# Kernel tuning notes

Hardware: AMD Instinct MI355X
Metric: run time of the kernel (lower is better)

The kernel has to match this reference:

```python
import jax, jax.numpy as jnp
import numpy as np

D_MODEL = 2048
D_COMPARE = 2048
D_MEMORY = 2048
N_HEADS = 16
KV_HEADS = 4
KV_REPEAT = N_HEADS // KV_HEADS          # 4
C_HD = D_COMPARE // N_HEADS              # 128 compare head dim
M_HD = D_MEMORY // N_HEADS               # 128 memory head dim
TOTAL_OUT = D_COMPARE + KV_HEADS * C_HD + KV_HEADS * M_HD  # 3072


def setup_inputs() -> dict:
    key = jax.random.key(0)
    ks = jax.random.split(key, 5)
    b, t = 2, 2048
    x = jax.random.normal(ks[0], (b, t, D_MODEL), dtype=jnp.float32)
    s_in = 1.0 / np.sqrt(D_MODEL)
    s_out = 1.0 / np.sqrt(D_MEMORY)
    in_w = jax.random.uniform(ks[1], (TOTAL_OUT, D_MODEL), jnp.float32, -s_in, s_in)
    in_b = jax.random.uniform(ks[2], (TOTAL_OUT,), jnp.float32, -s_in, s_in)
    out_w = jax.random.uniform(ks[3], (D_MODEL, D_MEMORY), jnp.float32, -s_out, s_out)
    out_b = jax.random.uniform(ks[4], (D_MODEL,), jnp.float32, -s_out, s_out)
    return {"x": x, "in_w": in_w, "in_b": in_b, "out_w": out_w, "out_b": out_b}


def reference(x, in_w, in_b, out_w, out_b):
    b, t, _ = x.shape
    packed = jnp.einsum("btd,od->bto", x, in_w) + in_b          # [b,t,TOTAL_OUT]
    q, k, v = jnp.split(packed, [D_COMPARE, D_COMPARE + KV_HEADS * C_HD], axis=-1)
    # q: [b, kv, rep, t, hd] -- head h maps to kv group h // KV_REPEAT
    # (torch repeat_interleave on KV head dim == grouped reshape of q heads)
    q = q.reshape(b, t, KV_HEADS, KV_REPEAT, C_HD).transpose(0, 2, 3, 1, 4)
    k = k.reshape(b, t, KV_HEADS, C_HD).transpose(0, 2, 1, 3)   # [b,kv,t,hd]
    v = v.reshape(b, t, KV_HEADS, M_HD).transpose(0, 2, 1, 3)   # [b,kv,t,mhd]
    scale = 1.0 / np.sqrt(C_HD)
    scores = jnp.einsum("bgrqd,bgkd->bgrqk", q, k) * scale      # [b,kv,rep,t,t]
    attn = jax.nn.softmax(scores, axis=-1)
    y = jnp.einsum("bgrqk,bgkd->bgrqd", attn, v)                # [b,kv,rep,t,mhd]
    y = y.transpose(0, 3, 1, 2, 4).reshape(b, t, D_MEMORY)      # heads back in order
    return jnp.einsum("btm,dm->btd", y, out_w) + out_b
```

## Files before the change

kernel.cpp:

```cpp
#include <hip/hip_runtime.h>
#include <hip/hip_bf16.h>
#include <stdint.h>

#define DEV __device__ __forceinline__

typedef __attribute__((ext_vector_type(8))) short bf16x8;
typedef __attribute__((ext_vector_type(4))) float f32x4;
typedef __attribute__((ext_vector_type(16))) float f32x16;
typedef __attribute__((ext_vector_type(4))) unsigned u32x4;

DEV unsigned short f2bf(float f) {
  unsigned u = __builtin_bit_cast(unsigned, f);
  unsigned r = u + 0x7FFF + ((u >> 16) & 1);
  return (unsigned short)(r >> 16);
}

DEV unsigned short f2bfh(float f) {
  __bf16 h = (__bf16)f;
  return __builtin_bit_cast(unsigned short, h);
}

DEV unsigned cvtpk(float lo, float hi) {
  unsigned r;
  asm("v_cvt_pk_bf16_f32 %0, %1, %2" : "=v"(r) : "v"(lo), "v"(hi));
  return r;
}

DEV void plswap(unsigned &a, unsigned &b) {
  asm("v_permlane32_swap_b32 %0, %1" : "+v"(a), "+v"(b));
}

typedef __attribute__((address_space(1))) void gvoid;
typedef __attribute__((address_space(3))) void lvoid;

DEV void g2l16(const void* g, void* l) {
  __builtin_amdgcn_global_load_lds((gvoid*)g, (lvoid*)l, 16, 0, 0);
}

#define MFMA16(a, b, c) __builtin_amdgcn_mfma_f32_16x16x32_bf16(a, b, c, 0, 0, 0)
#define MFMA32(a, b, c) __builtin_amdgcn_mfma_f32_32x32x16_bf16(a, b, c, 0, 0, 0)

__global__ void k_cvt3(const float* __restrict__ x, unsigned short* __restrict__ xo, int nx4,
                       const float* __restrict__ w, unsigned short* __restrict__ wo, int nw4,
                       const float* __restrict__ v, unsigned short* __restrict__ vo, int nv4) {
  int i = blockIdx.x * blockDim.x + threadIdx.x;
  int stride = gridDim.x * blockDim.x;
  int tot = nx4 + nw4 + nv4;
  for (; i < tot; i += stride) {
    const float* src; unsigned short* dst; int j = i;
    if (j < nx4) { src = x; dst = xo; }
    else if ((j -= nx4) < nw4) { src = w; dst = wo; }
    else { j -= nw4; src = v; dst = vo; }
    float4 val = reinterpret_cast<const float4*>(src)[j];
    ushort4 o;
    o.x = f2bf(val.x); o.y = f2bf(val.y); o.z = f2bf(val.z); o.w = f2bf(val.w);
    reinterpret_cast<ushort4*>(dst)[j] = o;
  }
}

template<bool BF16OUT>
__global__ __launch_bounds__(256, 2) void k_gemm(
    const unsigned short* __restrict__ A, const unsigned short* __restrict__ B,
    const float* __restrict__ bias, void* __restrict__ C,
    int M, int N, int K) {
  __shared__ unsigned short As[128 * 32];
  __shared__ unsigned short Bs[128 * 32];
  int tid = threadIdx.x;
  int lane = tid & 63, wid = tid >> 6;
  int bm = blockIdx.y * 128, bn = blockIdx.x * 128;
  int wm = (wid >> 1) * 64, wn = (wid & 1) * 64;
  int row16 = lane & 15, kq = lane >> 4;
  f32x4 acc[4][4] = {};
  int r = tid >> 2, c = (tid & 3) * 8;
  const unsigned short* Ag = A + (size_t)(bm + r) * K + c;
  const unsigned short* Bg = B + (size_t)(bn + r) * K + c;
  for (int k0 = 0; k0 < K; k0 += 32) {
    g2l16(Ag + k0, &As[tid * 8]);
    g2l16(Ag + (size_t)64 * K + k0, &As[2048 + tid * 8]);
    g2l16(Bg + k0, &Bs[tid * 8]);
    g2l16(Bg + (size_t)64 * K + k0, &Bs[2048 + tid * 8]);
    __syncthreads();
    bf16x8 a[4], b[4];
#pragma unroll
    for (int m = 0; m < 4; m++) a[m] = *(const bf16x8*)&As[(wm + m * 16 + row16) * 32 + kq * 8];
#pragma unroll
    for (int n = 0; n < 4; n++) b[n] = *(const bf16x8*)&Bs[(wn + n * 16 + row16) * 32 + kq * 8];
    __builtin_amdgcn_s_setprio(1);
#pragma unroll
    for (int m = 0; m < 4; m++)
#pragma unroll
      for (int n = 0; n < 4; n++)
        acc[m][n] = MFMA16(a[m], b[n], acc[m][n]);
    __builtin_amdgcn_s_setprio(0);
    __syncthreads();
  }
#pragma unroll
  for (int n = 0; n < 4; n++) {
    int col = bn + wn + n * 16 + row16;
    float bv = bias[col];
#pragma unroll
    for (int m = 0; m < 4; m++) {
      int rw = bm + wm + m * 16 + kq * 4;
#pragma unroll
      for (int j = 0; j < 4; j++) {
        float v = acc[m][n][j] + bv;
        if (BF16OUT) ((unsigned short*)C)[(size_t)(rw + j) * N + col] = f2bf(v);
        else         ((float*)C)[(size_t)(rw + j) * N + col] = v;
      }
    }
  }
}

__global__ void k_vt(const unsigned short* __restrict__ packed, unsigned short* __restrict__ vT) {
  __shared__ unsigned short tile[64][136];
  int g = blockIdx.y;
  int b = g >> 2, kv = g & 3;
  int t0 = blockIdx.x * 64;
  int tid = threadIdx.x;
#pragma unroll
  for (int i = 0; i < 4; i++) {
    int tl = i * 16 + (tid >> 4);
    int d0 = (tid & 15) * 8;
    bf16x8 v = *(const bf16x8*)&packed[(size_t)(b * 2048 + t0 + tl) * 3072 + 2560 + kv * 128 + d0];
    *(bf16x8*)&tile[tl][d0] = v;
  }
  __syncthreads();
  int d = tid >> 1, ts = (tid & 1) * 32;
  size_t obase = (size_t)(g * 128 + d) * 2048 + t0 + ts;
#pragma unroll
  for (int j = 0; j < 4; j++) {
    bf16x8 o;
#pragma unroll
    for (int e = 0; e < 8; e++) o[e] = (short)tile[ts + j * 8 + e][d];
    *(bf16x8*)&vT[obase + j * 8] = o;
  }
}

__global__ __launch_bounds__(256, 2) void k_flash(
    const unsigned short* __restrict__ packed,
    const unsigned short* __restrict__ vT,
    unsigned short* __restrict__ Y) {
  __shared__ unsigned short Ks[2][64 * 128];
  __shared__ unsigned short Vs[3][128 * 64];
  int tid = threadIdx.x, lane = tid & 63, wid = tid >> 6;
  int l31 = lane & 31, hi = lane >> 5;
  int kx = l31 & 15;
  int vx = l31 & 7;
  int g = blockIdx.x;
  int s8 = g & 7;
  int b = s8 >> 2, kv = s8 & 3;
  int w = g >> 3;
  int h = kv * 4 + (w & 3);
  int qt = w >> 2;
  size_t prow = (size_t)b * 2048;

  unsigned short* Q = &Ks[0][0];
  {
    int rr = tid >> 4;
    int cc = ((tid & 15) ^ rr) * 8;
    const unsigned short* qg = packed + (prow + qt * 128 + rr) * 3072 + h * 128 + cc;
#pragma unroll
    for (int i = 0; i < 8; i++)
      g2l16(qg + (size_t)i * 16 * 3072, &Q[i * 2048 + tid * 8]);
  }
  asm volatile("s_waitcnt vmcnt(0)" ::: "memory");
  __builtin_amdgcn_s_barrier();
  bf16x8 q[8];
  int qrow = wid * 32 + l31;
#pragma unroll
  for (int kc = 0; kc < 8; kc++)
    q[kc] = *(const bf16x8*)&Q[qrow * 128 + (((2 * kc + hi) ^ kx) * 8)];
  asm volatile("s_waitcnt lgkmcnt(0)" ::: "memory");
  __builtin_amdgcn_sched_barrier(0);
  __builtin_amdgcn_s_barrier();

  const unsigned short* kg0 = packed + prow * 3072 + 2048 + kv * 128;
  const unsigned short* vg0 = vT + (size_t)(b * 4 + kv) * 128 * 2048;
  int krr = tid >> 4;
  int kcc = ((tid & 15) ^ krr) * 8;
  int vrr = tid >> 3;
  int vcc = ((tid & 7) ^ (vrr & 7)) * 8;

  auto stageK = [&](int t, int buf) {
    const unsigned short* kg = kg0 + (size_t)(t * 64 + krr) * 3072 + kcc;
#pragma unroll
    for (int i = 0; i < 4; i++)
      g2l16(kg + (size_t)i * 16 * 3072, &Ks[buf][i * 2048 + tid * 8]);
  };
  auto stageV = [&](int t, int buf) {
    const unsigned short* vg = vg0 + (size_t)vrr * 2048 + t * 64 + vcc;
#pragma unroll
    for (int i = 0; i < 4; i++)
      g2l16(vg + (size_t)i * 32 * 2048, &Vs[buf][i * 2048 + tid * 8]);
  };

  auto qkt = [&](int kbuf, f32x16* stx) {
#pragma unroll
    for (int kb2 = 0; kb2 < 2; kb2++) {
      bf16x8 ak[8];
#pragma unroll
      for (int kc = 0; kc < 8; kc++)
        ak[kc] = *(const bf16x8*)&Ks[kbuf][(kb2 * 32 + l31) * 128 + (((2 * kc + hi) ^ kx) * 8)];
      __builtin_amdgcn_s_setprio(1);
#pragma unroll
      for (int kc = 0; kc < 8; kc++)
        stx[kb2] = MFMA32(ak[kc], q[kc], stx[kb2]);
      __builtin_amdgcn_s_setprio(0);
    }
  };

  stageK(0, 0); stageV(0, 0);
  stageK(1, 1); stageV(1, 1);
  asm volatile("s_waitcnt vmcnt(8)" ::: "memory");
  __builtin_amdgcn_s_barrier();

  f32x16 stc[2] = {};
  qkt(0, stc);
  asm volatile("s_waitcnt lgkmcnt(0)" ::: "memory");
  __builtin_amdgcn_sched_barrier(0);
  __builtin_amdgcn_s_barrier();

  f32x16 o[4] = {};
  f32x16 ls = {};
  const float sc2 = 0.08838834764831845f * 1.4426950408889634f;
  const float MOFF = 14.f;
  bf16x8 ones;
#pragma unroll
  for (int e = 0; e < 8; e++) ones[e] = (short)0x3F80;

  for (int t = 0; t < 32; t++) {
    int tn2 = t + 2 <= 31 ? t + 2 : 31;

    stageK(tn2, t & 1);
    stageV(tn2, (t + 2) % 3);

    f32x16 stn[2] = {};
    qkt((t + 1) & 1, stn);

#pragma unroll
    for (int kb2 = 0; kb2 < 2; kb2++)
#pragma unroll
      for (int r = 0; r < 16; r++)
        stc[kb2][r] = exp2f(fmaf(stc[kb2][r], sc2, -MOFF));

    bf16x8 pf[4];
#pragma unroll
    for (int kb2 = 0; kb2 < 2; kb2++) {
      unsigned E0 = cvtpk(stc[kb2][0],  stc[kb2][1]);
      unsigned E1 = cvtpk(stc[kb2][2],  stc[kb2][3]);
      unsigned E2 = cvtpk(stc[kb2][4],  stc[kb2][5]);
      unsigned E3 = cvtpk(stc[kb2][6],  stc[kb2][7]);
      unsigned E4 = cvtpk(stc[kb2][8],  stc[kb2][9]);
      unsigned E5 = cvtpk(stc[kb2][10], stc[kb2][11]);
      unsigned E6 = cvtpk(stc[kb2][12], stc[kb2][13]);
      unsigned E7 = cvtpk(stc[kb2][14], stc[kb2][15]);
      plswap(E0, E2); plswap(E1, E3);
      plswap(E4, E6); plswap(E5, E7);
      pf[2 * kb2 + 0] = __builtin_bit_cast(bf16x8, u32x4{E0, E1, E2, E3});
      pf[2 * kb2 + 1] = __builtin_bit_cast(bf16x8, u32x4{E4, E5, E6, E7});
    }

#pragma unroll
    for (int db = 0; db < 4; db++) {
      bf16x8 bv[4];
#pragma unroll
      for (int ks = 0; ks < 4; ks++)
        bv[ks] = *(const bf16x8*)&Vs[t % 3][(32 * db + l31) * 64 + (((2 * ks + hi) ^ vx) * 8)];
      __builtin_amdgcn_s_setprio(1);
#pragma unroll
      for (int ks = 0; ks < 4; ks++)
        o[db] = MFMA32(pf[ks], bv[ks], o[db]);
      __builtin_amdgcn_s_setprio(0);
    }
#pragma unroll
    for (int ks = 0; ks < 4; ks++)
      ls = MFMA32(pf[ks], ones, ls);

    stc[0] = stn[0];
    stc[1] = stn[1];

    asm volatile("s_waitcnt vmcnt(4)" ::: "memory");
    __builtin_amdgcn_s_barrier();
  }
  asm volatile("s_waitcnt vmcnt(0)" ::: "memory");

#pragma unroll
  for (int r = 0; r < 16; r++) {
    int ql = (r & 3) + 8 * (r >> 2) + 4 * hi;
    float inv = 1.f / ls[r];
    size_t orow = prow + (size_t)qt * 128 + wid * 32 + ql;
#pragma unroll
    for (int db = 0; db < 4; db++)
      Y[orow * 2048 + h * 128 + db * 32 + l31] = f2bfh(o[db][r] * inv);
  }
}

extern "C" void kernel_launch(void* const* d_in, const int* in_sizes, int n_in,
                              void* d_out, int out_size, void* d_ws, size_t ws_size,
                              hipStream_t stream) {
  const float* x     = (const float*)d_in[0];
  const float* in_w  = (const float*)d_in[1];
  const float* in_b  = (const float*)d_in[2];
  const float* out_w = (const float*)d_in[3];
  const float* out_b = (const float*)d_in[4];
  float* out = (float*)d_out;

  unsigned short* xb     = (unsigned short*)d_ws;
  unsigned short* wb     = xb + 8388608;
  unsigned short* owb    = wb + 6291456;
  unsigned short* packed = owb + 4194304;
  unsigned short* vt     = packed + 12582912;
  unsigned short* y      = vt + 2097152;

  k_cvt3<<<dim3(2048), dim3(256), 0, stream>>>(x, xb, 8388608 / 4,
                                               in_w, wb, 6291456 / 4,
                                               out_w, owb, 4194304 / 4);

  k_gemm<true><<<dim3(24, 32), dim3(256), 0, stream>>>(xb, wb, in_b, packed, 4096, 3072, 2048);
  k_vt<<<dim3(32, 8), dim3(256), 0, stream>>>(packed, vt);
  k_flash<<<dim3(512), dim3(256), 0, stream>>>(packed, vt, y);
  k_gemm<false><<<dim3(16, 32), dim3(256), 0, stream>>>(y, owb, out_b, out, 4096, 2048, 2048);
}
```

Before: 222.7 us.

## Pre-pack K/V into MFMA fragment order and stream directly into registers

Replaces the V-transpose kernel with a pack kernel that writes K and V tiles in exact per-lane MFMA fragment order into a workspace reusing the xb buffer. The flash kernel drops its LDS staging of K/V, the swizzled LDS reads and the vmcnt waits, and instead issues coalesced global loads straight into registers, prefetching the next fragments between MFMA groups. This removes LDS traffic and most synchronisation. In exchange each block re-reads K/V from L2/global with no LDS sharing across waves, and register pressure rises.

Result: no change. 222.3 us (-0.2%).

```diff
diff --git a/kernel.cpp b/kernel.cpp
--- a/kernel.cpp
+++ b/kernel.cpp
@@ -111,41 +111,52 @@
   }
 }
 
-__global__ void k_vt(const unsigned short* __restrict__ packed, unsigned short* __restrict__ vT) {
+__global__ void k_pack(const unsigned short* __restrict__ packed, unsigned short* __restrict__ attp) {
   __shared__ unsigned short tile[64][136];
-  int g = blockIdx.y;
+  int t = blockIdx.x, g = blockIdx.y;
   int b = g >> 2, kv = g & 3;
-  int t0 = blockIdx.x * 64;
   int tid = threadIdx.x;
 #pragma unroll
   for (int i = 0; i < 4; i++) {
     int tl = i * 16 + (tid >> 4);
     int d0 = (tid & 15) * 8;
-    bf16x8 v = *(const bf16x8*)&packed[(size_t)(b * 2048 + t0 + tl) * 3072 + 2560 + kv * 128 + d0];
-    *(bf16x8*)&tile[tl][d0] = v;
+    *(bf16x8*)&tile[tl][d0] =
+        *(const bf16x8*)&packed[(size_t)(b * 2048 + t * 64 + tl) * 3072 + 2560 + kv * 128 + d0];
+  }
+  size_t obase = (size_t)(g * 32 + t) * 32 * 64 * 8;
+#pragma unroll
+  for (int f = 0; f < 4; f++) {
+    int idx = f * 256 + tid;
+    int frag = idx >> 6, lane = idx & 63;
+    int l31 = lane & 31, h2 = lane >> 5;
+    int kb2 = frag >> 3, kc = frag & 7;
+    const unsigned short* src = &packed[(size_t)(b * 2048 + t * 64 + kb2 * 32 + l31) * 3072
+                                        + 2048 + kv * 128 + (2 * kc + h2) * 8];
+    *(bf16x8*)&attp[obase + (size_t)(frag * 64 + lane) * 8] = *(const bf16x8*)src;
   }
   __syncthreads();
-  int d = tid >> 1, ts = (tid & 1) * 32;
-  size_t obase = (size_t)(g * 128 + d) * 2048 + t0 + ts;
-#pragma unroll
-  for (int j = 0; j < 4; j++) {
-    bf16x8 o;
-#pragma unroll
-    for (int e = 0; e < 8; e++) o[e] = (short)tile[ts + j * 8 + e][d];
-    *(bf16x8*)&vT[obase + j * 8] = o;
+#pragma unroll
+  for (int f = 0; f < 4; f++) {
+    int idx = f * 256 + tid;
+    int f16 = idx >> 6, lane = idx & 63;
+    int l31 = lane & 31, h2 = lane >> 5;
+    int db = f16 >> 2, ks = f16 & 3;
+    int d = 32 * db + l31;
+    bf16x8 ov;
+#pragma unroll
+    for (int e = 0; e < 8; e++) ov[e] = (short)tile[(2 * ks + h2) * 8 + e][d];
+    *(bf16x8*)&attp[obase + (size_t)((16 + f16) * 64 + lane) * 8] = ov;
   }
 }
 
 __global__ __launch_bounds__(256, 2) void k_flash(
     const unsigned short* __restrict__ packed,
-    const unsigned short* __restrict__ vT,
+    const unsigned short* __restrict__ attp,
     unsigned short* __restrict__ Y) {
-  __shared__ unsigned short Ks[2][64 * 128];
-  __shared__ unsigned short Vs[3][128 * 64];
+  __shared__ unsigned short Qs[128 * 128];
   int tid = threadIdx.x, lane = tid & 63, wid = tid >> 6;
   int l31 = lane & 31, hi = lane >> 5;
   int kx = l31 & 15;
-  int vx = l31 & 7;
   int g = blockIdx.x;
   int s8 = g & 7;
   int b = s8 >> 2, kv = s8 & 3;
@@ -154,14 +165,13 @@
   int qt = w >> 2;
   size_t prow = (size_t)b * 2048;
 
-  unsigned short* Q = &Ks[0][0];
   {
     int rr = tid >> 4;
     int cc = ((tid & 15) ^ rr) * 8;
     const unsigned short* qg = packed + (prow + qt * 128 + rr) * 3072 + h * 128 + cc;
 #pragma unroll
     for (int i = 0; i < 8; i++)
-      g2l16(qg + (size_t)i * 16 * 3072, &Q[i * 2048 + tid * 8]);
+      g2l16(qg + (size_t)i * 16 * 3072, &Qs[i * 2048 + tid * 8]);
   }
   asm volatile("s_waitcnt vmcnt(0)" ::: "memory");
   __builtin_amdgcn_s_barrier();
@@ -169,56 +179,21 @@
   int qrow = wid * 32 + l31;
 #pragma unroll
   for (int kc = 0; kc < 8; kc++)
-    q[kc] = *(const bf16x8*)&Q[qrow * 128 + (((2 * kc + hi) ^ kx) * 8)];
+    q[kc] = *(const bf16x8*)&Qs[qrow * 128 + (((2 * kc + hi) ^ kx) * 8)];
   asm volatile("s_waitcnt lgkmcnt(0)" ::: "memory");
   __builtin_amdgcn_sched_barrier(0);
   __builtin_amdgcn_s_barrier();
 
-  const unsigned short* kg0 = packed + prow * 3072 + 2048 + kv * 128;
-  const unsigned short* vg0 = vT + (size_t)(b * 4 + kv) * 128 * 2048;
-  int krr = tid >> 4;
-  int kcc = ((tid & 15) ^ krr) * 8;
-  int vrr = tid >> 3;
-  int vcc = ((tid & 7) ^ (vrr & 7)) * 8;
-
-  auto stageK = [&](int t, int buf) {
-    const unsigned short* kg = kg0 + (size_t)(t * 64 + krr) * 3072 + kcc;
-#pragma unroll
-    for (int i = 0; i < 4; i++)
-      g2l16(kg + (size_t)i * 16 * 3072, &Ks[buf][i * 2048 + tid * 8]);
-  };
-  auto stageV = [&](int t, int buf) {
-    const unsigned short* vg = vg0 + (size_t)vrr * 2048 + t * 64 + vcc;
-#pragma unroll
-    for (int i = 0; i < 4; i++)
-      g2l16(vg + (size_t)i * 32 * 2048, &Vs[buf][i * 2048 + tid * 8]);
-  };
-
-  auto qkt = [&](int kbuf, f32x16* stx) {
-#pragma unroll
-    for (int kb2 = 0; kb2 < 2; kb2++) {
-      bf16x8 ak[8];
-#pragma unroll
-      for (int kc = 0; kc < 8; kc++)
-        ak[kc] = *(const bf16x8*)&Ks[kbuf][(kb2 * 32 + l31) * 128 + (((2 * kc + hi) ^ kx) * 8)];
-      __builtin_amdgcn_s_setprio(1);
-#pragma unroll
-      for (int kc = 0; kc < 8; kc++)
-        stx[kb2] = MFMA32(ak[kc], q[kc], stx[kb2]);
-      __builtin_amdgcn_s_setprio(0);
-    }
-  };
-
-  stageK(0, 0); stageV(0, 0);
-  stageK(1, 1); stageV(1, 1);
-  asm volatile("s_waitcnt vmcnt(8)" ::: "memory");
-  __builtin_amdgcn_s_barrier();
-
-  f32x16 stc[2] = {};
-  qkt(0, stc);
-  asm volatile("s_waitcnt lgkmcnt(0)" ::: "memory");
-  __builtin_amdgcn_sched_barrier(0);
-  __builtin_amdgcn_s_barrier();
+  const bf16x8* pk = (const bf16x8*)attp + ((size_t)s8 << 16);
+
+  bf16x8 b0[4], b1[4], b2[4], b3[4];
+#pragma unroll
+  for (int j = 0; j < 4; j++) {
+    b0[j] = pk[((0 + j) << 6) | lane];
+    b1[j] = pk[((4 + j) << 6) | lane];
+    b2[j] = pk[((8 + j) << 6) | lane];
+    b3[j] = pk[((12 + j) << 6) | lane];
+  }
 
   f32x16 o[4] = {};
   f32x16 ls = {};
@@ -229,60 +204,98 @@
   for (int e = 0; e < 8; e++) ones[e] = (short)0x3F80;
 
   for (int t = 0; t < 32; t++) {
-    int tn2 = t + 2 <= 31 ? t + 2 : 31;
-
-    stageK(tn2, t & 1);
-    stageV(tn2, (t + 2) % 3);
-
-    f32x16 stn[2] = {};
-    qkt((t + 1) & 1, stn);
-
-#pragma unroll
-    for (int kb2 = 0; kb2 < 2; kb2++)
-#pragma unroll
-      for (int r = 0; r < 16; r++)
-        stc[kb2][r] = exp2f(fmaf(stc[kb2][r], sc2, -MOFF));
+    const bf16x8* pt  = pk + ((size_t)t << 11);
+    const bf16x8* ptn = pk + ((size_t)(t < 31 ? t + 1 : 31) << 11);
+
+    f32x16 st0 = {}, st1 = {};
+    __builtin_amdgcn_s_setprio(1);
+#pragma unroll
+    for (int j = 0; j < 4; j++) st0 = MFMA32(b0[j], q[j], st0);
+    __builtin_amdgcn_s_setprio(0);
+#pragma unroll
+    for (int j = 0; j < 4; j++) b0[j] = pt[((16 + j) << 6) | lane];
+    __builtin_amdgcn_s_setprio(1);
+#pragma unroll
+    for (int j = 0; j < 4; j++) st0 = MFMA32(b1[j], q[4 + j], st0);
+    __builtin_amdgcn_s_setprio(0);
+#pragma unroll
+    for (int j = 0; j < 4; j++) b1[j] = pt[((20 + j) << 6) | lane];
+    __builtin_amdgcn_s_setprio(1);
+#pragma unroll
+    for (int j = 0; j < 4; j++) st1 = MFMA32(b2[j], q[j], st1);
+    __builtin_amdgcn_s_setprio(0);
+#pragma unroll
+    for (int j = 0; j < 4; j++) b2[j] = pt[((24 + j) << 6) | lane];
+    __builtin_amdgcn_s_setprio(1);
+#pragma unroll
+    for (int j = 0; j < 4; j++) st1 = MFMA32(b3[j], q[4 + j], st1);
+    __builtin_amdgcn_s_setprio(0);
+#pragma unroll
+    for (int j = 0; j < 4; j++) b3[j] = pt[((28 + j) << 6) | lane];
+
+#pragma unroll
+    for (int r = 0; r < 16; r++) st0[r] = exp2f(fmaf(st0[r], sc2, -MOFF));
+#pragma unroll
+    for (int r = 0; r < 16; r++) st1[r] = exp2f(fmaf(st1[r], sc2, -MOFF));
 
     bf16x8 pf[4];
-#pragma unroll
-    for (int kb2 = 0; kb2 < 2; kb2++) {
-      unsigned E0 = cvtpk(stc[kb2][0],  stc[kb2][1]);
-      unsigned E1 = cvtpk(stc[kb2][2],  stc[kb2][3]);
-      unsigned E2 = cvtpk(stc[kb2][4],  stc[kb2][5]);
-      unsigned E3 = cvtpk(stc[kb2][6],  stc[kb2][7]);
-      unsigned E4 = cvtpk(stc[kb2][8],  stc[kb2][9]);
-      unsigned E5 = cvtpk(stc[kb2][10], stc[kb2][11]);
-      unsigned E6 = cvtpk(stc[kb2][12], stc[kb2][13]);
-      unsigned E7 = cvtpk(stc[kb2][14], stc[kb2][15]);
+    {
+      unsigned E0 = cvtpk(st0[0],  st0[1]);
+      unsigned E1 = cvtpk(st0[2],  st0[3]);
+      unsigned E2 = cvtpk(st0[4],  st0[5]);
+      unsigned E3 = cvtpk(st0[6],  st0[7]);
+      unsigned E4 = cvtpk(st0[8],  st0[9]);
+      unsigned E5 = cvtpk(st0[10], st0[11]);
+      unsigned E6 = cvtpk(st0[12], st0[13]);
+      unsigned E7 = cvtpk(st0[14], st0[15]);
       plswap(E0, E2); plswap(E1, E3);
       plswap(E4, E6); plswap(E5, E7);
-      pf[2 * kb2 + 0] = __builtin_bit_cast(bf16x8, u32x4{E0, E1, E2, E3});
-      pf[2 * kb2 + 1] = __builtin_bit_cast(bf16x8, u32x4{E4, E5, E6, E7});
+      pf[0] = __builtin_bit_cast(bf16x8, u32x4{E0, E1, E2, E3});
+      pf[1] = __builtin_bit_cast(bf16x8, u32x4{E4, E5, E6, E7});
+      unsigned F0 = cvtpk(st1[0],  st1[1]);
+      unsigned F1 = cvtpk(st1[2],  st1[3]);
+      unsigned F2 = cvtpk(st1[4],  st1[5]);
+      unsigned F3 = cvtpk(st1[6],  st1[7]);
+      unsigned F4 = cvtpk(st1[8],  st1[9]);
+      unsigned F5 = cvtpk(st1[10], st1[11]);
+      unsigned F6 = cvtpk(st1[12], st1[13]);
+      unsigned F7 = cvtpk(st1[14], st1[15]);
+      plswap(F0, F2); plswap(F1, F3);
+      plswap(F4, F6); plswap(F5, F7);
+      pf[2] = __builtin_bit_cast(bf16x8, u32x4{F0, F1, F2, F3});
+      pf[3] = __builtin_bit_cast(bf16x8, u32x4{F4, F5, F6, F7});
     }
 
 #pragma unroll
-    for (int db = 0; db < 4; db++) {
-      bf16x8 bv[4];
-#pragma unroll
-      for (int ks = 0; ks < 4; ks++)
-        bv[ks] = *(const bf16x8*)&Vs[t % 3][(32 * db + l31) * 64 + (((2 * ks + hi) ^ vx) * 8)];
-      __builtin_amdgcn_s_setprio(1);
-#pragma unroll
-      for (int ks = 0; ks < 4; ks++)
-        o[db] = MFMA32(pf[ks], bv[ks], o[db]);
-      __builtin_amdgcn_s_setprio(0);
-    }
-#pragma unroll
-    for (int ks = 0; ks < 4; ks++)
-      ls = MFMA32(pf[ks], ones, ls);
-
-    stc[0] = stn[0];
-    stc[1] = stn[1];
-
-    asm volatile("s_waitcnt vmcnt(4)" ::: "memory");
+    for (int ks = 0; ks < 4; ks++) ls = MFMA32(pf[ks], ones, ls);
+
+    __builtin_amdgcn_s_setprio(1);
+#pragma unroll
+    for (int j = 0; j < 4; j++) o[0] = MFMA32(pf[j], b0[j], o[0]);
+    __builtin_amdgcn_s_setprio(0);
+#pragma unroll
+    for (int j = 0; j < 4; j++) b0[j] = ptn[((0 + j) << 6) | lane];
+    __builtin_amdgcn_s_setprio(1);
+#pragma unroll
+    for (int j = 0; j < 4; j++) o[1] = MFMA32(pf[j], b1[j], o[1]);
+    __builtin_amdgcn_s_setprio(0);
+#pragma unroll
+    for (int j = 0; j < 4; j++) b1[j] = ptn[((4 + j) << 6) | lane];
+    __builtin_amdgcn_s_setprio(1);
+#pragma unroll
+    for (int j = 0; j < 4; j++) o[2] = MFMA32(pf[j], b2[j], o[2]);
+    __builtin_amdgcn_s_setprio(0);
+#pragma unroll
+    for (int j = 0; j < 4; j++) b2[j] = ptn[((8 + j) << 6) | lane];
+    __builtin_amdgcn_s_setprio(1);
+#pragma unroll
+    for (int j = 0; j < 4; j++) o[3] = MFMA32(pf[j], b3[j], o[3]);
+    __builtin_amdgcn_s_setprio(0);
+#pragma unroll
+    for (int j = 0; j < 4; j++) b3[j] = ptn[((12 + j) << 6) | lane];
+
     __builtin_amdgcn_s_barrier();
   }
-  asm volatile("s_waitcnt vmcnt(0)" ::: "memory");
 
 #pragma unroll
   for (int r = 0; r < 16; r++) {
@@ -309,15 +322,15 @@
   unsigned short* wb     = xb + 8388608;
   unsigned short* owb    = wb + 6291456;
   unsigned short* packed = owb + 4194304;
-  unsigned short* vt     = packed + 12582912;
-  unsigned short* y      = vt + 2097152;
+  unsigned short* y      = packed + 12582912;
+  unsigned short* attp   = xb;
 
   k_cvt3<<<dim3(2048), dim3(256), 0, stream>>>(x, xb, 8388608 / 4,
                                                in_w, wb, 6291456 / 4,
                                                out_w, owb, 4194304 / 4);
 
   k_gemm<true><<<dim3(24, 32), dim3(256), 0, stream>>>(xb, wb, in_b, packed, 4096, 3072, 2048);
-  k_vt<<<dim3(32, 8), dim3(256), 0, stream>>>(packed, vt);
-  k_flash<<<dim3(512), dim3(256), 0, stream>>>(packed, vt, y);
+  k_pack<<<dim3(32, 8), dim3(256), 0, stream>>>(packed, attp);
+  k_flash<<<dim3(512), dim3(256), 0, stream>>>(packed, attp, y);
   k_gemm<false><<<dim3(16, 32), dim3(256), 0, stream>>>(y, owb, out_b, out, 4096, 2048, 2048);
 }
```
